# Optimization experiments

Measured on AMD Instinct MI355X. Metric: run time of the kernel, lower is better.

## Reference

```python
import jax, jax.numpy as jnp
import numpy as np

N_NODES = 100000
N_EDGES = 1600000
HIDDEN = 128
DENSE = 64
N_GRAPHS = 512


def setup_inputs() -> dict:
    key = jax.random.key(0)
    ks = jax.random.split(key, 12)
    x = jax.random.normal(ks[0], (N_NODES, 3), dtype=jnp.float32)
    edge_index = jax.random.randint(ks[1], (2, N_EDGES), 0, N_NODES, dtype=jnp.int64)
    batch = jnp.sort(jax.random.randint(ks[2], (N_NODES,), 0, N_GRAPHS, dtype=jnp.int64))
    def lin(k, fan_in, fan_out):
        s = 1.0 / np.sqrt(fan_in)
        kw, kb = jax.random.split(k)
        W = jax.random.uniform(kw, (fan_in, fan_out), jnp.float32, -s, s)
        b = jax.random.uniform(kb, (fan_out,), jnp.float32, -s, s)
        return W, b
    W0, b0 = lin(ks[3], 3, HIDDEN)
    W1, b1 = lin(ks[4], HIDDEN, HIDDEN)
    W2, b2 = lin(ks[5], HIDDEN, HIDDEN)
    Wf1, bf1 = lin(ks[6], HIDDEN, DENSE)
    Wf2, bf2 = lin(ks[7], DENSE, 1)
    return {"x": x, "edge_index": edge_index, "batch": batch,
            "W0": W0, "b0": b0, "W1": W1, "b1": b1, "W2": W2, "b2": b2,
            "Wf1": Wf1, "bf1": bf1, "Wf2": Wf2, "bf2": bf2}


def reference(x, edge_index, batch, W0, b0, W1, b1, W2, b2, Wf1, bf1, Wf2, bf2):
    N = x.shape[0]
    loop = jnp.arange(N, dtype=edge_index.dtype)
    src = jnp.concatenate([edge_index[0], loop])  # [E+N] with self-loops
    dst = jnp.concatenate([edge_index[1], loop])
    deg = jax.ops.segment_sum(jnp.ones_like(dst, dtype=x.dtype), dst, num_segments=N)
    dis = jax.lax.rsqrt(jnp.maximum(deg, 1.0))  # D^{-1/2}; self-loops => deg >= 1
    norm = dis[src] * dis[dst]  # [E+N]

    def gcn_conv(h, W, b):
        h = h @ W  # transform first (PyG GCNConv)
        msg = h[src] * norm[:, None]  # gather + edge-wise scale
        return jax.ops.segment_sum(msg, dst, num_segments=N) + b  # scatter-add

    h = jax.nn.relu(gcn_conv(x, W0, b0))
    h = jax.nn.relu(gcn_conv(h, W1, b1))
    h = jax.nn.relu(gcn_conv(h, W2, b2))

    # global mean pool over graphs
    counts = jax.ops.segment_sum(jnp.ones((N,), h.dtype), batch, num_segments=N_GRAPHS)
    pooled = jax.ops.segment_sum(h, batch, num_segments=N_GRAPHS)
    pooled = pooled / jnp.maximum(counts, 1.0)[:, None]  # [G, HIDDEN]

    out = jax.nn.relu(pooled @ Wf1 + bf1)
    return out @ Wf2 + bf2  # [G, 1]
```

## Files before the change

kernel.cpp:

```cpp
#include <hip/hip_runtime.h>

#define HID 128
#define ELLW 64
#define FP8_SCALE 16.0f
#define FP8_INV (1.0f / 16.0f)

#define NBINS 400
#define BINCAP 16
#define CHUNK_I4 512
#define BKCAP 5120
#define OVF_CAP 16384

typedef _Float16 half8 __attribute__((ext_vector_type(8)));
typedef float f32x4 __attribute__((ext_vector_type(4)));
typedef float f32x2 __attribute__((ext_vector_type(2)));
struct alignas(8) H4v { _Float16 x, y, z, w; };

__device__ __forceinline__ unsigned char f32_to_fp8(float v) {
  return (unsigned char)(__builtin_amdgcn_cvt_pk_fp8_f32(v, 0.f, 0, false) & 0xff);
}

__device__ __forceinline__ void fp8x8_to_f32(uint2 u, float* o) {
  f32x2 a = __builtin_amdgcn_cvt_pk_f32_fp8(u.x, false);
  f32x2 b = __builtin_amdgcn_cvt_pk_f32_fp8(u.x, true);
  f32x2 c = __builtin_amdgcn_cvt_pk_f32_fp8(u.y, false);
  f32x2 d = __builtin_amdgcn_cvt_pk_f32_fp8(u.y, true);
  o[0] = a[0]; o[1] = a[1]; o[2] = b[0]; o[3] = b[1];
  o[4] = c[0]; o[5] = c[1]; o[6] = d[0]; o[7] = d[1];
}

__device__ __forceinline__ void fp8x8_add(uint2 u, float* acc) {
  f32x2 a = __builtin_amdgcn_cvt_pk_f32_fp8(u.x, false);
  f32x2 b = __builtin_amdgcn_cvt_pk_f32_fp8(u.x, true);
  f32x2 c = __builtin_amdgcn_cvt_pk_f32_fp8(u.y, false);
  f32x2 d = __builtin_amdgcn_cvt_pk_f32_fp8(u.y, true);
  acc[0] += a[0]; acc[1] += a[1]; acc[2] += b[0]; acc[3] += b[1];
  acc[4] += c[0]; acc[5] += c[1]; acc[6] += d[0]; acc[7] += d[1];
}


__global__ void k_zero_ints(int* p, int n) {
  int i = blockIdx.x * blockDim.x + threadIdx.x;
  if (i < n) p[i] = 0;
}

__device__ __forceinline__ void bin_one(int s, int d, int* lcnt, unsigned* bins,
                                        int* ovfn, int2* ovf) {
  int b = d >> 8;
  int p = atomicAdd(&lcnt[b], 1);
  if (p < BINCAP) bins[b * BINCAP + p] = ((unsigned)s << 8) | (unsigned)(d & 255);
  else { int q = atomicAdd(ovfn, 1); if (q < OVF_CAP) ovf[q] = make_int2(s, d); }
}

__global__ __launch_bounds__(256) void k_binA(
    const int4* __restrict__ src4, const int4* __restrict__ dst4, int E4,
    int* bkcnt, unsigned* __restrict__ bk, int* ovfn, int2* __restrict__ ovf) {
  __shared__ unsigned bins[NBINS * BINCAP];
  __shared__ int lcnt[NBINS];
  __shared__ int gbase[NBINS];
  int t = threadIdx.x;
  for (int b = t; b < NBINS; b += 256) lcnt[b] = 0;
  __syncthreads();

  int i0 = blockIdx.x * CHUNK_I4;
  int i1 = min(i0 + CHUNK_I4, E4);
  for (int i = i0 + t; i < i1; i += 256) {
    int4 d = dst4[i];
    int4 s = src4[i];
    bin_one(s.x, d.x, lcnt, bins, ovfn, ovf);
    bin_one(s.y, d.y, lcnt, bins, ovfn, ovf);
    bin_one(s.z, d.z, lcnt, bins, ovfn, ovf);
    bin_one(s.w, d.w, lcnt, bins, ovfn, ovf);
  }
  __syncthreads();

  for (int b = t; b < NBINS; b += 256) gbase[b] = atomicAdd(&bkcnt[b], min(lcnt[b], BINCAP));
  __syncthreads();

  int wid = t >> 6, lane = t & 63;
  for (int b = wid; b < NBINS; b += 4) {
    int c = min(lcnt[b], BINCAP);
    if (lane < c) {
      int off = gbase[b] + lane;
      unsigned r = bins[b * BINCAP + lane];
      if (off < BKCAP) bk[(size_t)b * BKCAP + off] = r;
      else {
        int q = atomicAdd(ovfn, 1);
        if (q < OVF_CAP) ovf[q] = make_int2((int)(r >> 8), b * 256 + (int)(r & 255));
      }
    }
  }
}

__global__ void k_tail_ovf(const int* __restrict__ src, const int* __restrict__ dst,
                           int e0, int E, int* ovfn, int2* __restrict__ ovf) {
  int e = e0 + threadIdx.x;
  if (e < E) {
    int q = atomicAdd(ovfn, 1);
    if (q < OVF_CAP) ovf[q] = make_int2(src[e], dst[e]);
  }
}


__global__ __launch_bounds__(256) void k_ell_build2(
    const unsigned* __restrict__ bk, const int* __restrict__ bkcnt,
    int* __restrict__ ell, int* __restrict__ cnt,
    const float* __restrict__ x, float* __restrict__ dis,
    float4* __restrict__ x4, int N) {
  int b = blockIdx.x;
  int t = threadIdx.x;
  __shared__ int lcnt[256];
  lcnt[t] = 0;
  __syncthreads();
  int n = bkcnt[b]; if (n > BKCAP) n = BKCAP;
  const unsigned* my = bk + (size_t)b * BKCAP;
  for (int k = t; k < n; k += 256) {
    unsigned r = my[k];
    int d0 = (int)(r & 255);
    int s = (int)(r >> 8);
    int p = atomicAdd(&lcnt[d0], 1);
    if (p < ELLW) ell[(size_t)(b * 256 + d0) * ELLW + p] = s;
  }
  __syncthreads();
  int node = b * 256 + t;
  if (node < N) {
    int c = lcnt[t];
    cnt[node] = c;
    float s = rsqrtf((float)(c + 1));
    dis[node] = s;
    x4[node] = make_float4(s * x[node * 3 + 0], s * x[node * 3 + 1],
                           s * x[node * 3 + 2], 0.f);
  }
}

__global__ void k_ovf_build(const int2* __restrict__ ovf, const int* __restrict__ ovfn,
                            int* cnt, int* ell, const float* __restrict__ x,
                            float* dis, float4* x4) {
  int n = *ovfn; if (n > OVF_CAP) n = OVF_CAP;
  for (int k = threadIdx.x; k < n; k += blockDim.x) {
    int2 e = ovf[k];
    int p = atomicAdd(&cnt[e.y], 1);
    if (p < ELLW) ell[(size_t)e.y * ELLW + p] = e.x;
  }
  __syncthreads();
  for (int k = threadIdx.x; k < n; k += blockDim.x) {
    int d = ovf[k].y;
    float s = rsqrtf((float)(cnt[d] + 1));
    dis[d] = s;
    x4[d] = make_float4(s * x[d * 3 + 0], s * x[d * 3 + 1], s * x[d * 3 + 2], 0.f);
  }
}


__global__ void k_fill_ell1(const int* __restrict__ src, const int* __restrict__ dst,
                            int* cnt, int* ell, int E) {
  int e = blockIdx.x * blockDim.x + threadIdx.x;
  if (e < E) {
    int d = dst[e];
    int p = atomicAdd(&cnt[d], 1);
    if (p < ELLW) ell[(size_t)d * ELLW + p] = src[e];
  }
}

__global__ void k_dis_prepx(const int* __restrict__ cnt, const float* __restrict__ x,
                            float* __restrict__ dis, float4* __restrict__ x4, int N) {
  int i = blockIdx.x * blockDim.x + threadIdx.x;
  if (i >= N) return;
  float s = rsqrtf((float)(cnt[i] + 1));
  dis[i] = s;
  x4[i] = make_float4(s * x[i * 3 + 0], s * x[i * 3 + 1], s * x[i * 3 + 2], 0.f);
}


__global__ void k_prep_w16x2(const float* __restrict__ W1, const float* __restrict__ W2,
                             _Float16* __restrict__ Wt1, _Float16* __restrict__ Wt2) {
  int idx = blockIdx.x * blockDim.x + threadIdx.x;
  if (idx >= 2 * HID * HID) return;
  int which = idx >> 14;
  int r = idx & (HID * HID - 1);
  int k = r >> 7, n = r & 127;
  const float* W = which ? W2 : W1;
  _Float16* Wt = which ? Wt2 : Wt1;
  Wt[n * HID + k] = (_Float16)W[r];
}


__global__ void k_agg3(const float4* __restrict__ x4, const int* __restrict__ ell,
                       const int* __restrict__ cnt, const float* __restrict__ dis,
                       float4* __restrict__ z4, int N) {
  int i = blockIdx.x * blockDim.x + threadIdx.x;
  if (i >= N) return;
  float4 a = x4[i];
  int c = cnt[i]; if (c > ELLW) c = ELLW;
  const int* row = &ell[(size_t)i * ELLW];
  int k = 0;
  for (; k + 4 <= c; k += 4) {
    int4 s4 = *(const int4*)(row + k);
    float4 v0 = x4[s4.x], v1 = x4[s4.y], v2 = x4[s4.z], v3 = x4[s4.w];
    a.x += (v0.x + v1.x) + (v2.x + v3.x);
    a.y += (v0.y + v1.y) + (v2.y + v3.y);
    a.z += (v0.z + v1.z) + (v2.z + v3.z);
  }
  for (; k < c; ++k) {
    float4 v = x4[row[k]];
    a.x += v.x; a.y += v.y; a.z += v.z;
  }
  float s = dis[i];
  z4[i] = make_float4(s * a.x, s * a.y, s * a.z, 0.f);
}


__global__ __launch_bounds__(256) void k_l01(
    const float4* __restrict__ z4, const float* __restrict__ W0,
    const float* __restrict__ b0, const _Float16* __restrict__ wt1,
    const float* __restrict__ dis, unsigned char* __restrict__ G8, int N) {
  __shared__ _Float16 hs[64][136];
  int t = threadIdx.x;
  int base = blockIdx.x * 64;

  {
    int r = t >> 2;
    int c0 = (t & 3) * 32;
    int row = base + r;
    float4 z = make_float4(0.f, 0.f, 0.f, 0.f);
    if (row < N) z = z4[row];
#pragma unroll
    for (int c = 0; c < 32; c += 4) {
      int cc = c0 + c;
      float4 w0 = *(const float4*)&W0[0 * HID + cc];
      float4 w1 = *(const float4*)&W0[1 * HID + cc];
      float4 w2 = *(const float4*)&W0[2 * HID + cc];
      float4 bb = *(const float4*)&b0[cc];
      H4v o;
      o.x = (_Float16)fmaxf(z.x * w0.x + z.y * w1.x + z.z * w2.x + bb.x, 0.f);
      o.y = (_Float16)fmaxf(z.x * w0.y + z.y * w1.y + z.z * w2.y + bb.y, 0.f);
      o.z = (_Float16)fmaxf(z.x * w0.z + z.y * w1.z + z.z * w2.z + bb.z, 0.f);
      o.w = (_Float16)fmaxf(z.x * w0.w + z.y * w1.w + z.z * w2.w + bb.w, 0.f);
      *(H4v*)&hs[r][cc] = o;
    }
  }
  __syncthreads();

  int w = t >> 6, lane = t & 63;
  int kg = lane >> 4, ccol = lane & 15;
  int lrow = w * 16 + ccol;

  f32x4 acc[8];
#pragma unroll
  for (int nt = 0; nt < 8; ++nt) acc[nt] = (f32x4){0.f, 0.f, 0.f, 0.f};

#pragma unroll
  for (int kt = 0; kt < 4; ++kt) {
    half8 a = *(const half8*)&hs[lrow][kg * 8 + kt * 32];
#pragma unroll
    for (int nt = 0; nt < 8; ++nt) {
      half8 b = *(const half8*)(wt1 + (size_t)(nt * 16 + ccol) * HID + kg * 8 + kt * 32);
      acc[nt] = __builtin_amdgcn_mfma_f32_16x16x32_f16(a, b, acc[nt], 0, 0, 0);
    }
  }

#pragma unroll
  for (int j = 0; j < 4; ++j) {
    int row = base + w * 16 + kg * 4 + j;
    if (row < N) {
      float s = dis[row] * FP8_SCALE;
#pragma unroll
      for (int nt = 0; nt < 8; ++nt) {
        G8[(size_t)row * HID + nt * 16 + ccol] = f32_to_fp8(s * acc[nt][j]);
      }
    }
  }
}


__global__ __launch_bounds__(256) void k_g1(
    const unsigned char* __restrict__ g8, const int* __restrict__ ell,
    const int* __restrict__ cnt, const float* __restrict__ dis,
    const float* __restrict__ b, unsigned char* __restrict__ q8, int N) {
  int tid = blockIdx.x * blockDim.x + threadIdx.x;
  int i = tid >> 4;
  int q = tid & 15;
  if (i >= N) return;
  const unsigned char* gq = g8 + q * 8;

  float acc[8];
  fp8x8_to_f32(*(const uint2*)(gq + (size_t)i * HID), acc);

  int c = cnt[i]; if (c > ELLW) c = ELLW;
  const int* row = ell + (size_t)i * ELLW;
  int k = 0;
  for (; k + 4 <= c; k += 4) {
    int4 s4 = *(const int4*)(row + k);
    uint2 u0 = *(const uint2*)(gq + (size_t)s4.x * HID);
    uint2 u1 = *(const uint2*)(gq + (size_t)s4.y * HID);
    uint2 u2 = *(const uint2*)(gq + (size_t)s4.z * HID);
    uint2 u3 = *(const uint2*)(gq + (size_t)s4.w * HID);
    fp8x8_add(u0, acc);
    fp8x8_add(u1, acc);
    fp8x8_add(u2, acc);
    fp8x8_add(u3, acc);
  }
  for (; k < c; ++k) {
    fp8x8_add(*(const uint2*)(gq + (size_t)row[k] * HID), acc);
  }

  float sc = dis[i];
  float sc_in = sc * FP8_INV;
  float sc_out = sc * FP8_SCALE;
  float o[8];
#pragma unroll
  for (int j = 0; j < 8; ++j) {
    float bb = b[q * 8 + j];
    o[j] = sc_out * fmaxf(sc_in * acc[j] + bb, 0.f);
  }
  int w0 = __builtin_amdgcn_cvt_pk_fp8_f32(o[0], o[1], 0, false);
  w0 = __builtin_amdgcn_cvt_pk_fp8_f32(o[2], o[3], w0, true);
  int w1 = __builtin_amdgcn_cvt_pk_fp8_f32(o[4], o[5], 0, false);
  w1 = __builtin_amdgcn_cvt_pk_fp8_f32(o[6], o[7], w1, true);
  uint2 ov; ov.x = (unsigned)w0; ov.y = (unsigned)w1;
  *(uint2*)(q8 + (size_t)i * HID + q * 8) = ov;
}


__global__ __launch_bounds__(256) void k_gpool2(
    const unsigned char* __restrict__ q8, const int* __restrict__ ell,
    const int* __restrict__ cnt, const float* __restrict__ dis,
    const float* __restrict__ b2, const _Float16* __restrict__ wt2,
    const int* __restrict__ batch, float* __restrict__ pool, int N) {
  __shared__ _Float16 hs[16][136];
  int t = threadIdx.x;
  int base = blockIdx.x * 16;
  int gi = t >> 4, q = t & 15;
  int i = base + gi;

  if (i < N) {
    const unsigned char* gq = q8 + q * 8;
    float acc[8];
    fp8x8_to_f32(*(const uint2*)(gq + (size_t)i * HID), acc);

    int c = cnt[i]; if (c > ELLW) c = ELLW;
    const int* row = ell + (size_t)i * ELLW;
    int k = 0;
    for (; k + 4 <= c; k += 4) {
      int4 s4 = *(const int4*)(row + k);
      uint2 u0 = *(const uint2*)(gq + (size_t)s4.x * HID);
      uint2 u1 = *(const uint2*)(gq + (size_t)s4.y * HID);
      uint2 u2 = *(const uint2*)(gq + (size_t)s4.z * HID);
      uint2 u3 = *(const uint2*)(gq + (size_t)s4.w * HID);
      fp8x8_add(u0, acc);
      fp8x8_add(u1, acc);
      fp8x8_add(u2, acc);
      fp8x8_add(u3, acc);
    }
    for (; k < c; ++k) {
      fp8x8_add(*(const uint2*)(gq + (size_t)row[k] * HID), acc);
    }

    float sc = dis[i] * FP8_INV;
    half8 o;
#pragma unroll
    for (int j = 0; j < 8; ++j) o[j] = (_Float16)(sc * acc[j]);
    *(half8*)&hs[gi][q * 8] = o;
  } else {
    half8 zo;
#pragma unroll
    for (int j = 0; j < 8; ++j) zo[j] = (_Float16)0.f;
    *(half8*)&hs[gi][q * 8] = zo;
  }
  __syncthreads();

  int w = t >> 6, lane = t & 63;
  int kg = lane >> 4, rloc = lane & 15;
  f32x4 acc2[2];
  acc2[0] = (f32x4){0.f, 0.f, 0.f, 0.f};
  acc2[1] = (f32x4){0.f, 0.f, 0.f, 0.f};

#pragma unroll
  for (int kt = 0; kt < 4; ++kt) {
    half8 a = *(const half8*)&hs[rloc][kg * 8 + kt * 32];
#pragma unroll
    for (int ntl = 0; ntl < 2; ++ntl) {
      int n = (2 * w + ntl) * 16 + rloc;
      half8 bf = *(const half8*)(wt2 + (size_t)n * HID + kg * 8 + kt * 32);
      acc2[ntl] = __builtin_amdgcn_mfma_f32_16x16x32_f16(a, bf, acc2[ntl], 0, 0, 0);
    }
  }

  float v2[2][4];
#pragma unroll
  for (int ntl = 0; ntl < 2; ++ntl) {
    int col = (2 * w + ntl) * 16 + rloc;
    float bb = b2[col];
#pragma unroll
    for (int j = 0; j < 4; ++j) v2[ntl][j] = fmaxf(acc2[ntl][j] + bb, 0.f);
  }
  int brow[4];
#pragma unroll
  for (int j = 0; j < 4; ++j) {
    int row = base + kg * 4 + j;
    brow[j] = (row < N) ? batch[row] : -1;
  }
  int g0 = batch[base];
  int lastr = base + 15; if (lastr >= N) lastr = N - 1;
  int g1 = batch[lastr];

  for (int s = g0; s <= g1; ++s) {
#pragma unroll
    for (int ntl = 0; ntl < 2; ++ntl) {
      float p = 0.f;
#pragma unroll
      for (int j = 0; j < 4; ++j) p += (brow[j] == s) ? v2[ntl][j] : 0.f;
      p += __shfl_xor(p, 16);
      p += __shfl_xor(p, 32);
      if (kg == 0 && p != 0.f) {
        atomicAdd(&pool[s * HID + (2 * w + ntl) * 16 + rloc], p);
      }
    }
  }
}


__device__ __forceinline__ int lower_bound_i(const int* __restrict__ a, int n, int v) {
  int lo = 0, hi = n;
  while (lo < hi) {
    int m = (lo + hi) >> 1;
    if (a[m] < v) lo = m + 1; else hi = m;
  }
  return lo;
}

__global__ __launch_bounds__(64) void k_mlp512(
    const float* __restrict__ pool, const int* __restrict__ batch, int N,
    const float* __restrict__ Wf1, const float* __restrict__ bf1,
    const float* __restrict__ Wf2, const float* __restrict__ bf2,
    float* __restrict__ out) {
  int g = blockIdx.x;
  int lane = threadIdx.x;
  int lo = lower_bound_i(batch, N, g);
  int hi = lower_bound_i(batch, N, g + 1);
  float inv = 1.0f / fmaxf((float)(hi - lo), 1.0f);

  __shared__ float p[128];
  p[lane] = pool[g * HID + lane] * inv;
  p[lane + 64] = pool[g * HID + 64 + lane] * inv;
  __syncthreads();

  float a = bf1[lane];
  for (int k = 0; k < 128; ++k) a += p[k] * Wf1[k * 64 + lane];
  a = fmaxf(a, 0.f);
  float prod = a * Wf2[lane];
#pragma unroll
  for (int off = 32; off; off >>= 1) prod += __shfl_down(prod, off);
  if (lane == 0) out[g] = prod + bf2[0];
}


static inline size_t align256(size_t x) { return (x + 255) & ~(size_t)255; }

extern "C" void kernel_launch(void* const* d_in, const int* in_sizes, int n_in,
                              void* d_out, int out_size, void* d_ws, size_t ws_size,
                              hipStream_t stream) {
  const float* x = (const float*)d_in[0];
  const int* ei = (const int*)d_in[1];
  const int* batch = (const int*)d_in[2];
  const float* W0 = (const float*)d_in[3];
  const float* b0 = (const float*)d_in[4];
  const float* W1 = (const float*)d_in[5];
  const float* b1 = (const float*)d_in[6];
  const float* W2 = (const float*)d_in[7];
  const float* b2 = (const float*)d_in[8];
  const float* Wf1 = (const float*)d_in[9];
  const float* bf1 = (const float*)d_in[10];
  const float* Wf2 = (const float*)d_in[11];
  const float* bf2 = (const float*)d_in[12];
  float* out = (float*)d_out;

  const int N = in_sizes[0] / 3;
  const int E = in_sizes[1] / 2;
  const int Gn = out_size;
  const int nbuk = (N + 255) >> 8;

  const int* src = ei;
  const int* dst = ei + E;

  char* ws = (char*)d_ws;
  size_t o = 0;
  int* cnt = (int*)(ws + o); o = align256(o + (size_t)N * 4);
  float* dis = (float*)(ws + o); o = align256(o + (size_t)N * 4);
  float4* x4 = (float4*)(ws + o); o = align256(o + (size_t)N * 16);
  float4* z4 = (float4*)(ws + o); o = align256(o + (size_t)N * 16);
  int* ell = (int*)(ws + o); o = align256(o + (size_t)N * ELLW * 4);
  unsigned char* g8a = (unsigned char*)(ws + o); o = align256(o + (size_t)N * HID);
  unsigned char* q8 = (unsigned char*)(ws + o); o = align256(o + (size_t)N * HID);
  _Float16* wt1 = (_Float16*)(ws + o); o = align256(o + (size_t)HID * HID * 2);
  _Float16* wt2 = (_Float16*)(ws + o); o = align256(o + (size_t)HID * HID * 2);
  size_t zero_base = o;
  int* bkcnt = (int*)(ws + o); o = align256(o + (size_t)(NBINS + 1) * 4);
  int* ovfn = bkcnt + NBINS;
  float* pool = (float*)(ws + o); o = align256(o + (size_t)Gn * HID * 4);
  size_t zero_bytes = o - zero_base;
  unsigned* bk = (unsigned*)(ws + o); o = align256(o + (size_t)NBINS * BKCAP * 4);
  int2* ovf = (int2*)(ws + o); o = align256(o + (size_t)OVF_CAP * 8);

  const int BS = 256;
  int gN = (N + BS - 1) / BS;
  int gN16 = (int)(((long long)N * 16 + BS - 1) / BS);
  int gW2 = (2 * HID * HID + BS - 1) / BS;
  int zn = (int)(zero_bytes / 4);

  k_zero_ints<<<(zn + BS - 1) / BS, BS, 0, stream>>>((int*)(ws + zero_base), zn);

  bool vec4ok = (E % 4 == 0) && (((uintptr_t)src & 15) == 0) && (((uintptr_t)dst & 15) == 0);
  if (nbuk <= NBINS) {
    int E4 = E / 4;
    if (E4 > 0 && vec4ok) {
      k_binA<<<(E4 + CHUNK_I4 - 1) / CHUNK_I4, 256, 0, stream>>>(
          (const int4*)src, (const int4*)dst, E4, bkcnt, bk, ovfn, ovf);
      if (E % 4) k_tail_ovf<<<1, 64, 0, stream>>>(src, dst, E4 * 4, E, ovfn, ovf);
    } else {
      k_tail_ovf<<<1, 256, 0, stream>>>(src, dst, 0, E, ovfn, ovf);
    }
    k_ell_build2<<<nbuk, 256, 0, stream>>>(bk, bkcnt, ell, cnt, x, dis, x4, N);
    k_ovf_build<<<1, 256, 0, stream>>>(ovf, ovfn, cnt, ell, x, dis, x4);
  } else {
    k_zero_ints<<<gN, BS, 0, stream>>>(cnt, N);
    k_fill_ell1<<<(E + BS - 1) / BS, BS, 0, stream>>>(src, dst, cnt, ell, E);
    k_dis_prepx<<<gN, BS, 0, stream>>>(cnt, x, dis, x4, N);
  }

  k_prep_w16x2<<<gW2, BS, 0, stream>>>(W1, W2, wt1, wt2);

  k_agg3<<<gN, BS, 0, stream>>>(x4, ell, cnt, dis, z4, N);

  k_l01<<<(N + 63) / 64, 256, 0, stream>>>(z4, W0, b0, wt1, dis, g8a, N);

  k_g1<<<gN16, BS, 0, stream>>>(g8a, ell, cnt, dis, b1, q8, N);

  k_gpool2<<<(N + 15) / 16, 256, 0, stream>>>(q8, ell, cnt, dis, b2, wt2, batch, pool, N);

  k_mlp512<<<Gn, 64, 0, stream>>>(pool, batch, N, Wf1, bf1, Wf2, bf2, out);
}
```

Measured before the change: 234.9 us.

## Rebalance per-node thread mapping in aggregation kernels with wider fp8 gathers

The first-layer aggregation now uses four threads per node with strided neighbor loops and a shuffle reduction, instead of one thread per node. The fp8 gather kernels for layers 1 and 2 use eight threads per node, each loading 16 bytes, instead of sixteen threads loading 8 bytes. The pool kernel processes 32 nodes per block, with each wave computing four MFMA column tiles. The aim is to spread irregular degree work more evenly for the 3-wide features and to halve the number of gather instructions per row. The cost is more registers per thread and fewer threads in flight for the 128-wide layers.

```diff
diff --git a/kernel.cpp b/kernel.cpp
--- a/kernel.cpp
+++ b/kernel.cpp
@@ -18,15 +18,6 @@
 
 __device__ __forceinline__ unsigned char f32_to_fp8(float v) {
   return (unsigned char)(__builtin_amdgcn_cvt_pk_fp8_f32(v, 0.f, 0, false) & 0xff);
-}
-
-__device__ __forceinline__ void fp8x8_to_f32(uint2 u, float* o) {
-  f32x2 a = __builtin_amdgcn_cvt_pk_f32_fp8(u.x, false);
-  f32x2 b = __builtin_amdgcn_cvt_pk_f32_fp8(u.x, true);
-  f32x2 c = __builtin_amdgcn_cvt_pk_f32_fp8(u.y, false);
-  f32x2 d = __builtin_amdgcn_cvt_pk_f32_fp8(u.y, true);
-  o[0] = a[0]; o[1] = a[1]; o[2] = b[0]; o[3] = b[1];
-  o[4] = c[0]; o[5] = c[1]; o[6] = d[0]; o[7] = d[1];
 }
 
 __device__ __forceinline__ void fp8x8_add(uint2 u, float* acc) {
@@ -36,6 +27,26 @@
   f32x2 d = __builtin_amdgcn_cvt_pk_f32_fp8(u.y, true);
   acc[0] += a[0]; acc[1] += a[1]; acc[2] += b[0]; acc[3] += b[1];
   acc[4] += c[0]; acc[5] += c[1]; acc[6] += d[0]; acc[7] += d[1];
+}
+
+__device__ __forceinline__ void fp8x16_to_f32(uint4 u, float* o) {
+  f32x2 a = __builtin_amdgcn_cvt_pk_f32_fp8(u.x, false);
+  f32x2 b = __builtin_amdgcn_cvt_pk_f32_fp8(u.x, true);
+  f32x2 c = __builtin_amdgcn_cvt_pk_f32_fp8(u.y, false);
+  f32x2 d = __builtin_amdgcn_cvt_pk_f32_fp8(u.y, true);
+  f32x2 e = __builtin_amdgcn_cvt_pk_f32_fp8(u.z, false);
+  f32x2 f = __builtin_amdgcn_cvt_pk_f32_fp8(u.z, true);
+  f32x2 g = __builtin_amdgcn_cvt_pk_f32_fp8(u.w, false);
+  f32x2 h = __builtin_amdgcn_cvt_pk_f32_fp8(u.w, true);
+  o[0]=a[0]; o[1]=a[1]; o[2]=b[0]; o[3]=b[1];
+  o[4]=c[0]; o[5]=c[1]; o[6]=d[0]; o[7]=d[1];
+  o[8]=e[0]; o[9]=e[1]; o[10]=f[0]; o[11]=f[1];
+  o[12]=g[0]; o[13]=g[1]; o[14]=h[0]; o[15]=h[1];
+}
+
+__device__ __forceinline__ void fp8x16_add(uint4 u, float* acc) {
+  fp8x8_add(make_uint2(u.x, u.y), acc);
+  fp8x8_add(make_uint2(u.z, u.w), acc + 8);
 }
 
 
@@ -188,25 +199,27 @@
 __global__ void k_agg3(const float4* __restrict__ x4, const int* __restrict__ ell,
                        const int* __restrict__ cnt, const float* __restrict__ dis,
                        float4* __restrict__ z4, int N) {
-  int i = blockIdx.x * blockDim.x + threadIdx.x;
+  int tid = blockIdx.x * blockDim.x + threadIdx.x;
+  int i = tid >> 2, sub = tid & 3;
   if (i >= N) return;
-  float4 a = x4[i];
+  float ax = 0.f, ay = 0.f, az = 0.f;
   int c = cnt[i]; if (c > ELLW) c = ELLW;
   const int* row = &ell[(size_t)i * ELLW];
-  int k = 0;
-  for (; k + 4 <= c; k += 4) {
-    int4 s4 = *(const int4*)(row + k);
-    float4 v0 = x4[s4.x], v1 = x4[s4.y], v2 = x4[s4.z], v3 = x4[s4.w];
-    a.x += (v0.x + v1.x) + (v2.x + v3.x);
-    a.y += (v0.y + v1.y) + (v2.y + v3.y);
-    a.z += (v0.z + v1.z) + (v2.z + v3.z);
-  }
-  for (; k < c; ++k) {
+  for (int k = sub; k < c; k += 4) {
     float4 v = x4[row[k]];
-    a.x += v.x; a.y += v.y; a.z += v.z;
-  }
-  float s = dis[i];
-  z4[i] = make_float4(s * a.x, s * a.y, s * a.z, 0.f);
+    ax += v.x; ay += v.y; az += v.z;
+  }
+  if (sub == 0) {
+    float4 v = x4[i];
+    ax += v.x; ay += v.y; az += v.z;
+  }
+  ax += __shfl_xor(ax, 1); ax += __shfl_xor(ax, 2);
+  ay += __shfl_xor(ay, 1); ay += __shfl_xor(ay, 2);
+  az += __shfl_xor(az, 1); az += __shfl_xor(az, 2);
+  if (sub == 0) {
+    float s = dis[i];
+    z4[i] = make_float4(s * ax, s * ay, s * az, 0.f);
+  }
 }
 
 
@@ -278,47 +291,52 @@
     const int* __restrict__ cnt, const float* __restrict__ dis,
     const float* __restrict__ b, unsigned char* __restrict__ q8, int N) {
   int tid = blockIdx.x * blockDim.x + threadIdx.x;
-  int i = tid >> 4;
-  int q = tid & 15;
+  int i = tid >> 3;
+  int q = tid & 7;
   if (i >= N) return;
-  const unsigned char* gq = g8 + q * 8;
-
-  float acc[8];
-  fp8x8_to_f32(*(const uint2*)(gq + (size_t)i * HID), acc);
+  const unsigned char* gq = g8 + q * 16;
+
+  float acc[16];
+  fp8x16_to_f32(*(const uint4*)(gq + (size_t)i * HID), acc);
 
   int c = cnt[i]; if (c > ELLW) c = ELLW;
   const int* row = ell + (size_t)i * ELLW;
   int k = 0;
   for (; k + 4 <= c; k += 4) {
     int4 s4 = *(const int4*)(row + k);
-    uint2 u0 = *(const uint2*)(gq + (size_t)s4.x * HID);
-    uint2 u1 = *(const uint2*)(gq + (size_t)s4.y * HID);
-    uint2 u2 = *(const uint2*)(gq + (size_t)s4.z * HID);
-    uint2 u3 = *(const uint2*)(gq + (size_t)s4.w * HID);
-    fp8x8_add(u0, acc);
-    fp8x8_add(u1, acc);
-    fp8x8_add(u2, acc);
-    fp8x8_add(u3, acc);
+    uint4 u0 = *(const uint4*)(gq + (size_t)s4.x * HID);
+    uint4 u1 = *(const uint4*)(gq + (size_t)s4.y * HID);
+    uint4 u2 = *(const uint4*)(gq + (size_t)s4.z * HID);
+    uint4 u3 = *(const uint4*)(gq + (size_t)s4.w * HID);
+    fp8x16_add(u0, acc);
+    fp8x16_add(u1, acc);
+    fp8x16_add(u2, acc);
+    fp8x16_add(u3, acc);
   }
   for (; k < c; ++k) {
-    fp8x8_add(*(const uint2*)(gq + (size_t)row[k] * HID), acc);
+    fp8x16_add(*(const uint4*)(gq + (size_t)row[k] * HID), acc);
   }
 
   float sc = dis[i];
   float sc_in = sc * FP8_INV;
   float sc_out = sc * FP8_SCALE;
-  float o[8];
-#pragma unroll
-  for (int j = 0; j < 8; ++j) {
-    float bb = b[q * 8 + j];
+  float o[16];
+#pragma unroll
+  for (int j = 0; j < 16; ++j) {
+    float bb = b[q * 16 + j];
     o[j] = sc_out * fmaxf(sc_in * acc[j] + bb, 0.f);
   }
+  uint4 ov;
   int w0 = __builtin_amdgcn_cvt_pk_fp8_f32(o[0], o[1], 0, false);
   w0 = __builtin_amdgcn_cvt_pk_fp8_f32(o[2], o[3], w0, true);
   int w1 = __builtin_amdgcn_cvt_pk_fp8_f32(o[4], o[5], 0, false);
   w1 = __builtin_amdgcn_cvt_pk_fp8_f32(o[6], o[7], w1, true);
-  uint2 ov; ov.x = (unsigned)w0; ov.y = (unsigned)w1;
-  *(uint2*)(q8 + (size_t)i * HID + q * 8) = ov;
+  int w2 = __builtin_amdgcn_cvt_pk_fp8_f32(o[8], o[9], 0, false);
+  w2 = __builtin_amdgcn_cvt_pk_fp8_f32(o[10], o[11], w2, true);
+  int w3 = __builtin_amdgcn_cvt_pk_fp8_f32(o[12], o[13], 0, false);
+  w3 = __builtin_amdgcn_cvt_pk_fp8_f32(o[14], o[15], w3, true);
+  ov.x = (unsigned)w0; ov.y = (unsigned)w1; ov.z = (unsigned)w2; ov.w = (unsigned)w3;
+  *(uint4*)(q8 + (size_t)i * HID + q * 16) = ov;
 }
 
 
@@ -327,69 +345,77 @@
     const int* __restrict__ cnt, const float* __restrict__ dis,
     const float* __restrict__ b2, const _Float16* __restrict__ wt2,
     const int* __restrict__ batch, float* __restrict__ pool, int N) {
-  __shared__ _Float16 hs[16][136];
+  __shared__ _Float16 hs[32][136];
   int t = threadIdx.x;
-  int base = blockIdx.x * 16;
-  int gi = t >> 4, q = t & 15;
+  int base = blockIdx.x * 32;
+  int gi = t >> 3, q = t & 7;
   int i = base + gi;
 
   if (i < N) {
-    const unsigned char* gq = q8 + q * 8;
-    float acc[8];
-    fp8x8_to_f32(*(const uint2*)(gq + (size_t)i * HID), acc);
+    const unsigned char* gq = q8 + q * 16;
+    float acc[16];
+    fp8x16_to_f32(*(const uint4*)(gq + (size_t)i * HID), acc);
 
     int c = cnt[i]; if (c > ELLW) c = ELLW;
     const int* row = ell + (size_t)i * ELLW;
     int k = 0;
     for (; k + 4 <= c; k += 4) {
       int4 s4 = *(const int4*)(row + k);
-      uint2 u0 = *(const uint2*)(gq + (size_t)s4.x * HID);
-      uint2 u1 = *(const uint2*)(gq + (size_t)s4.y * HID);
-      uint2 u2 = *(const uint2*)(gq + (size_t)s4.z * HID);
-      uint2 u3 = *(const uint2*)(gq + (size_t)s4.w * HID);
-      fp8x8_add(u0, acc);
-      fp8x8_add(u1, acc);
-      fp8x8_add(u2, acc);
-      fp8x8_add(u3, acc);
+      uint4 u0 = *(const uint4*)(gq + (size_t)s4.x * HID);
+      uint4 u1 = *(const uint4*)(gq + (size_t)s4.y * HID);
+      uint4 u2 = *(const uint4*)(gq + (size_t)s4.z * HID);
+      uint4 u3 = *(const uint4*)(gq + (size_t)s4.w * HID);
+      fp8x16_add(u0, acc);
+      fp8x16_add(u1, acc);
+      fp8x16_add(u2, acc);
+      fp8x16_add(u3, acc);
     }
     for (; k < c; ++k) {
-      fp8x8_add(*(const uint2*)(gq + (size_t)row[k] * HID), acc);
+      fp8x16_add(*(const uint4*)(gq + (size_t)row[k] * HID), acc);
     }
 
     float sc = dis[i] * FP8_INV;
-    half8 o;
-#pragma unroll
-    for (int j = 0; j < 8; ++j) o[j] = (_Float16)(sc * acc[j]);
-    *(half8*)&hs[gi][q * 8] = o;
+    half8 o0, o1;
+#pragma unroll
+    for (int j = 0; j < 8; ++j) {
+      o0[j] = (_Float16)(sc * acc[j]);
+      o1[j] = (_Float16)(sc * acc[8 + j]);
+    }
+    *(half8*)&hs[gi][q * 16] = o0;
+    *(half8*)&hs[gi][q * 16 + 8] = o1;
   } else {
     half8 zo;
 #pragma unroll
     for (int j = 0; j < 8; ++j) zo[j] = (_Float16)0.f;
-    *(half8*)&hs[gi][q * 8] = zo;
+    *(half8*)&hs[gi][q * 16] = zo;
+    *(half8*)&hs[gi][q * 16 + 8] = zo;
   }
   __syncthreads();
 
   int w = t >> 6, lane = t & 63;
   int kg = lane >> 4, rloc = lane & 15;
-  f32x4 acc2[2];
-  acc2[0] = (f32x4){0.f, 0.f, 0.f, 0.f};
-  acc2[1] = (f32x4){0.f, 0.f, 0.f, 0.f};
+  int tw = w >> 1, ch = w & 1;
+  int rbase = base + tw * 16;
+
+  f32x4 acc2[4];
+#pragma unroll
+  for (int ntl = 0; ntl < 4; ++ntl) acc2[ntl] = (f32x4){0.f, 0.f, 0.f, 0.f};
 
 #pragma unroll
   for (int kt = 0; kt < 4; ++kt) {
-    half8 a = *(const half8*)&hs[rloc][kg * 8 + kt * 32];
-#pragma unroll
-    for (int ntl = 0; ntl < 2; ++ntl) {
-      int n = (2 * w + ntl) * 16 + rloc;
+    half8 a = *(const half8*)&hs[tw * 16 + rloc][kg * 8 + kt * 32];
+#pragma unroll
+    for (int ntl = 0; ntl < 4; ++ntl) {
+      int n = (ch * 4 + ntl) * 16 + rloc;
       half8 bf = *(const half8*)(wt2 + (size_t)n * HID + kg * 8 + kt * 32);
       acc2[ntl] = __builtin_amdgcn_mfma_f32_16x16x32_f16(a, bf, acc2[ntl], 0, 0, 0);
     }
   }
 
-  float v2[2][4];
-#pragma unroll
-  for (int ntl = 0; ntl < 2; ++ntl) {
-    int col = (2 * w + ntl) * 16 + rloc;
+  float v2[4][4];
+#pragma unroll
+  for (int ntl = 0; ntl < 4; ++ntl) {
+    int col = (ch * 4 + ntl) * 16 + rloc;
     float bb = b2[col];
 #pragma unroll
     for (int j = 0; j < 4; ++j) v2[ntl][j] = fmaxf(acc2[ntl][j] + bb, 0.f);
@@ -397,23 +423,24 @@
   int brow[4];
 #pragma unroll
   for (int j = 0; j < 4; ++j) {
-    int row = base + kg * 4 + j;
+    int row = rbase + kg * 4 + j;
     brow[j] = (row < N) ? batch[row] : -1;
   }
-  int g0 = batch[base];
-  int lastr = base + 15; if (lastr >= N) lastr = N - 1;
+  int r0c = (rbase < N) ? rbase : (N - 1);
+  int lastr = rbase + 15; if (lastr >= N) lastr = N - 1;
+  int g0 = batch[r0c];
   int g1 = batch[lastr];
 
   for (int s = g0; s <= g1; ++s) {
 #pragma unroll
-    for (int ntl = 0; ntl < 2; ++ntl) {
+    for (int ntl = 0; ntl < 4; ++ntl) {
       float p = 0.f;
 #pragma unroll
       for (int j = 0; j < 4; ++j) p += (brow[j] == s) ? v2[ntl][j] : 0.f;
       p += __shfl_xor(p, 16);
       p += __shfl_xor(p, 32);
       if (kg == 0 && p != 0.f) {
-        atomicAdd(&pool[s * HID + (2 * w + ntl) * 16 + rloc], p);
+        atomicAdd(&pool[s * HID + (ch * 4 + ntl) * 16 + rloc], p);
       }
     }
   }
@@ -504,7 +531,8 @@
 
   const int BS = 256;
   int gN = (N + BS - 1) / BS;
-  int gN16 = (int)(((long long)N * 16 + BS - 1) / BS);
+  int gN4 = (int)(((long long)N * 4 + BS - 1) / BS);
+  int gN8 = (int)(((long long)N * 8 + BS - 1) / BS);
   int gW2 = (2 * HID * HID + BS - 1) / BS;
   int zn = (int)(zero_bytes / 4);
 
@@ -530,13 +558,13 @@
 
   k_prep_w16x2<<<gW2, BS, 0, stream>>>(W1, W2, wt1, wt2);
 
-  k_agg3<<<gN, BS, 0, stream>>>(x4, ell, cnt, dis, z4, N);
+  k_agg3<<<gN4, BS, 0, stream>>>(x4, ell, cnt, dis, z4, N);
 
   k_l01<<<(N + 63) / 64, 256, 0, stream>>>(z4, W0, b0, wt1, dis, g8a, N);
 
-  k_g1<<<gN16, BS, 0, stream>>>(g8a, ell, cnt, dis, b1, q8, N);
-
-  k_gpool2<<<(N + 15) / 16, 256, 0, stream>>>(q8, ell, cnt, dis, b2, wt2, batch, pool, N);
+  k_g1<<<gN8, BS, 0, stream>>>(g8a, ell, cnt, dis, b1, q8, N);
+
+  k_gpool2<<<(N + 31) / 32, 256, 0, stream>>>(q8, ell, cnt, dis, b2, wt2, batch, pool, N);
 
   k_mlp512<<<Gn, 64, 0, stream>>>(pool, batch, N, Wf1, bf1, Wf2, bf2, out);
 }
```

New measurement: 235.5 us. Within noise of the previous version (+0.3%).

## Aggregate first layer from dst buckets with LDS atomics; stage fp8 output for coalesced stores

Applied to the files above, without the earlier changes.

The first-layer 3-wide aggregation now runs directly over the destination-binned edge buckets. It accumulates into shared-memory atomics per 256-node bucket, plus a separate pass that adds overflow edges with global atomics, replacing the ELL row gather kernel. k_l01 now writes its fp8 outputs into LDS first and then stores 16-byte coalesced rows, instead of scattered byte stores. The trade-offs are LDS atomic contention, float atomic ordering nondeterminism, and extra syncthreads.

```diff
diff --git a/kernel.cpp b/kernel.cpp
--- a/kernel.cpp
+++ b/kernel.cpp
@@ -152,6 +152,51 @@
 }
 
 
+__global__ __launch_bounds__(256) void k_aggB(
+    const unsigned* __restrict__ bk, const int* __restrict__ bkcnt,
+    const float4* __restrict__ x4, const float* __restrict__ dis,
+    float4* __restrict__ z4, int N) {
+  __shared__ float sx[256], sy[256], sz[256];
+  int b = blockIdx.x;
+  int t = threadIdx.x;
+  sx[t] = 0.f; sy[t] = 0.f; sz[t] = 0.f;
+  __syncthreads();
+  int n = bkcnt[b]; if (n > BKCAP) n = BKCAP;
+  const unsigned* my = bk + (size_t)b * BKCAP;
+  for (int k = t; k < n; k += 256) {
+    unsigned r = my[k];
+    int d0 = (int)(r & 255);
+    float4 v = x4[r >> 8];
+    atomicAdd(&sx[d0], v.x);
+    atomicAdd(&sy[d0], v.y);
+    atomicAdd(&sz[d0], v.z);
+  }
+  __syncthreads();
+  int node = b * 256 + t;
+  if (node < N) {
+    float4 self = x4[node];
+    float s = dis[node];
+    z4[node] = make_float4(s * (sx[t] + self.x), s * (sy[t] + self.y),
+                           s * (sz[t] + self.z), 0.f);
+  }
+}
+
+__global__ void k_ovf_agg(const int2* __restrict__ ovf, const int* __restrict__ ovfn,
+                          const float* __restrict__ dis, const float4* __restrict__ x4,
+                          float4* z4) {
+  int n = *ovfn; if (n > OVF_CAP) n = OVF_CAP;
+  for (int k = threadIdx.x; k < n; k += blockDim.x) {
+    int2 e = ovf[k];
+    float4 v = x4[e.x];
+    float s = dis[e.y];
+    float* zp = (float*)&z4[e.y];
+    atomicAdd(zp + 0, s * v.x);
+    atomicAdd(zp + 1, s * v.y);
+    atomicAdd(zp + 2, s * v.z);
+  }
+}
+
+
 __global__ void k_fill_ell1(const int* __restrict__ src, const int* __restrict__ dst,
                             int* cnt, int* ell, int E) {
   int e = blockIdx.x * blockDim.x + threadIdx.x;
@@ -170,20 +215,6 @@
   dis[i] = s;
   x4[i] = make_float4(s * x[i * 3 + 0], s * x[i * 3 + 1], s * x[i * 3 + 2], 0.f);
 }
-
-
-__global__ void k_prep_w16x2(const float* __restrict__ W1, const float* __restrict__ W2,
-                             _Float16* __restrict__ Wt1, _Float16* __restrict__ Wt2) {
-  int idx = blockIdx.x * blockDim.x + threadIdx.x;
-  if (idx >= 2 * HID * HID) return;
-  int which = idx >> 14;
-  int r = idx & (HID * HID - 1);
-  int k = r >> 7, n = r & 127;
-  const float* W = which ? W2 : W1;
-  _Float16* Wt = which ? Wt2 : Wt1;
-  Wt[n * HID + k] = (_Float16)W[r];
-}
-
 
 __global__ void k_agg3(const float4* __restrict__ x4, const int* __restrict__ ell,
                        const int* __restrict__ cnt, const float* __restrict__ dis,
@@ -210,6 +241,19 @@
 }
 
 
+__global__ void k_prep_w16x2(const float* __restrict__ W1, const float* __restrict__ W2,
+                             _Float16* __restrict__ Wt1, _Float16* __restrict__ Wt2) {
+  int idx = blockIdx.x * blockDim.x + threadIdx.x;
+  if (idx >= 2 * HID * HID) return;
+  int which = idx >> 14;
+  int r = idx & (HID * HID - 1);
+  int k = r >> 7, n = r & 127;
+  const float* W = which ? W2 : W1;
+  _Float16* Wt = which ? Wt2 : Wt1;
+  Wt[n * HID + k] = (_Float16)W[r];
+}
+
+
 __global__ __launch_bounds__(256) void k_l01(
     const float4* __restrict__ z4, const float* __restrict__ W0,
     const float* __restrict__ b0, const _Float16* __restrict__ wt1,
@@ -258,16 +302,29 @@
       acc[nt] = __builtin_amdgcn_mfma_f32_16x16x32_f16(a, b, acc[nt], 0, 0, 0);
     }
   }
-
+  __syncthreads();
+
+  unsigned char* bytebuf = (unsigned char*)&hs[0][0];
 #pragma unroll
   for (int j = 0; j < 4; ++j) {
-    int row = base + w * 16 + kg * 4 + j;
+    int rl = w * 16 + kg * 4 + j;
+    int row = base + rl;
+    float s = dis[(row < N) ? row : (N - 1)] * FP8_SCALE;
+#pragma unroll
+    for (int nt = 0; nt < 8; ++nt) {
+      bytebuf[rl * 144 + nt * 16 + ccol] = f32_to_fp8(s * acc[nt][j]);
+    }
+  }
+  __syncthreads();
+
+#pragma unroll
+  for (int half = 0; half < 2; ++half) {
+    int rl = (t >> 3) + half * 32;
+    int seg = t & 7;
+    int row = base + rl;
     if (row < N) {
-      float s = dis[row] * FP8_SCALE;
-#pragma unroll
-      for (int nt = 0; nt < 8; ++nt) {
-        G8[(size_t)row * HID + nt * 16 + ccol] = f32_to_fp8(s * acc[nt][j]);
-      }
+      uint4 v = *(const uint4*)&bytebuf[rl * 144 + seg * 16];
+      *(uint4*)&G8[(size_t)row * HID + seg * 16] = v;
     }
   }
 }
@@ -522,16 +579,17 @@
     }
     k_ell_build2<<<nbuk, 256, 0, stream>>>(bk, bkcnt, ell, cnt, x, dis, x4, N);
     k_ovf_build<<<1, 256, 0, stream>>>(ovf, ovfn, cnt, ell, x, dis, x4);
+    k_aggB<<<nbuk, 256, 0, stream>>>(bk, bkcnt, x4, dis, z4, N);
+    k_ovf_agg<<<1, 256, 0, stream>>>(ovf, ovfn, dis, x4, z4);
   } else {
     k_zero_ints<<<gN, BS, 0, stream>>>(cnt, N);
     k_fill_ell1<<<(E + BS - 1) / BS, BS, 0, stream>>>(src, dst, cnt, ell, E);
     k_dis_prepx<<<gN, BS, 0, stream>>>(cnt, x, dis, x4, N);
+    k_agg3<<<gN, BS, 0, stream>>>(x4, ell, cnt, dis, z4, N);
   }
 
   k_prep_w16x2<<<gW2, BS, 0, stream>>>(W1, W2, wt1, wt2);
 
-  k_agg3<<<gN, BS, 0, stream>>>(x4, ell, cnt, dis, z4, N);
-
   k_l01<<<(N + 63) / 64, 256, 0, stream>>>(z4, W0, b0, wt1, dis, g8a, N);
 
   k_g1<<<gN16, BS, 0, stream>>>(g8a, ell, cnt, dis, b1, q8, N);
```

Result: slower. 253.3 us (+7.9%).

## Split layer-0 aggregation across four lanes per node and stage FP8 stores through LDS

Applied to the files above, without the earlier changes.

The first-layer 3-wide aggregation now gives each node four threads, one float component each, with an 8-way unrolled gather. This exposes more memory-level parallelism than one thread per node doing float4 gathers. Separately, k_l01 writes its FP8 outputs into shared memory and then copies them out as coalesced 16-byte rows, replacing scattered single-byte global stores. The cost is extra threads doing redundant index loads, plus additional barriers and LDS traffic in k_l01.

```diff
diff --git a/kernel.cpp b/kernel.cpp
--- a/kernel.cpp
+++ b/kernel.cpp
@@ -172,6 +172,45 @@
 }
 
 
+__global__ __launch_bounds__(256) void k_aggv(
+    const float* __restrict__ x4f, const int* __restrict__ ell,
+    const int* __restrict__ cnt, const float* __restrict__ dis,
+    float* __restrict__ z4f, int N) {
+  int tid = blockIdx.x * blockDim.x + threadIdx.x;
+  int i = tid >> 2, q = tid & 3;
+  if (i >= N) return;
+
+  float acc = x4f[i * 4 + q];
+  int c = cnt[i]; if (c > ELLW) c = ELLW;
+  const int* row = ell + (size_t)i * ELLW;
+  int k = 0;
+  for (; k + 8 <= c; k += 8) {
+    int4 sa = *(const int4*)(row + k);
+    int4 sb = *(const int4*)(row + k + 4);
+    float v0 = x4f[sa.x * 4 + q];
+    float v1 = x4f[sa.y * 4 + q];
+    float v2 = x4f[sa.z * 4 + q];
+    float v3 = x4f[sa.w * 4 + q];
+    float v4 = x4f[sb.x * 4 + q];
+    float v5 = x4f[sb.y * 4 + q];
+    float v6 = x4f[sb.z * 4 + q];
+    float v7 = x4f[sb.w * 4 + q];
+    acc += ((v0 + v1) + (v2 + v3)) + ((v4 + v5) + (v6 + v7));
+  }
+  for (; k + 4 <= c; k += 4) {
+    int4 s4 = *(const int4*)(row + k);
+    float v0 = x4f[s4.x * 4 + q];
+    float v1 = x4f[s4.y * 4 + q];
+    float v2 = x4f[s4.z * 4 + q];
+    float v3 = x4f[s4.w * 4 + q];
+    acc += (v0 + v1) + (v2 + v3);
+  }
+  for (; k < c; ++k) acc += x4f[row[k] * 4 + q];
+
+  z4f[i * 4 + q] = dis[i] * acc;
+}
+
+
 __global__ void k_prep_w16x2(const float* __restrict__ W1, const float* __restrict__ W2,
                              _Float16* __restrict__ Wt1, _Float16* __restrict__ Wt2) {
   int idx = blockIdx.x * blockDim.x + threadIdx.x;
@@ -182,31 +221,6 @@
   const float* W = which ? W2 : W1;
   _Float16* Wt = which ? Wt2 : Wt1;
   Wt[n * HID + k] = (_Float16)W[r];
-}
-
-
-__global__ void k_agg3(const float4* __restrict__ x4, const int* __restrict__ ell,
-                       const int* __restrict__ cnt, const float* __restrict__ dis,
-                       float4* __restrict__ z4, int N) {
-  int i = blockIdx.x * blockDim.x + threadIdx.x;
-  if (i >= N) return;
-  float4 a = x4[i];
-  int c = cnt[i]; if (c > ELLW) c = ELLW;
-  const int* row = &ell[(size_t)i * ELLW];
-  int k = 0;
-  for (; k + 4 <= c; k += 4) {
-    int4 s4 = *(const int4*)(row + k);
-    float4 v0 = x4[s4.x], v1 = x4[s4.y], v2 = x4[s4.z], v3 = x4[s4.w];
-    a.x += (v0.x + v1.x) + (v2.x + v3.x);
-    a.y += (v0.y + v1.y) + (v2.y + v3.y);
-    a.z += (v0.z + v1.z) + (v2.z + v3.z);
-  }
-  for (; k < c; ++k) {
-    float4 v = x4[row[k]];
-    a.x += v.x; a.y += v.y; a.z += v.z;
-  }
-  float s = dis[i];
-  z4[i] = make_float4(s * a.x, s * a.y, s * a.z, 0.f);
 }
 
 
@@ -258,16 +272,29 @@
       acc[nt] = __builtin_amdgcn_mfma_f32_16x16x32_f16(a, b, acc[nt], 0, 0, 0);
     }
   }
-
+  __syncthreads();
+
+  unsigned char* bytebuf = (unsigned char*)&hs[0][0];
 #pragma unroll
   for (int j = 0; j < 4; ++j) {
-    int row = base + w * 16 + kg * 4 + j;
+    int rl = w * 16 + kg * 4 + j;
+    int row = base + rl;
+    float s = dis[(row < N) ? row : (N - 1)] * FP8_SCALE;
+#pragma unroll
+    for (int nt = 0; nt < 8; ++nt) {
+      bytebuf[rl * 144 + nt * 16 + ccol] = f32_to_fp8(s * acc[nt][j]);
+    }
+  }
+  __syncthreads();
+
+#pragma unroll
+  for (int half = 0; half < 2; ++half) {
+    int rl = (t >> 3) + half * 32;
+    int seg = t & 7;
+    int row = base + rl;
     if (row < N) {
-      float s = dis[row] * FP8_SCALE;
-#pragma unroll
-      for (int nt = 0; nt < 8; ++nt) {
-        G8[(size_t)row * HID + nt * 16 + ccol] = f32_to_fp8(s * acc[nt][j]);
-      }
+      uint4 v = *(const uint4*)&bytebuf[rl * 144 + seg * 16];
+      *(uint4*)&G8[(size_t)row * HID + seg * 16] = v;
     }
   }
 }
@@ -504,6 +531,7 @@
 
   const int BS = 256;
   int gN = (N + BS - 1) / BS;
+  int gN4 = (int)(((long long)N * 4 + BS - 1) / BS);
   int gN16 = (int)(((long long)N * 16 + BS - 1) / BS);
   int gW2 = (2 * HID * HID + BS - 1) / BS;
   int zn = (int)(zero_bytes / 4);
@@ -528,10 +556,10 @@
     k_dis_prepx<<<gN, BS, 0, stream>>>(cnt, x, dis, x4, N);
   }
 
+  k_aggv<<<gN4, BS, 0, stream>>>((const float*)x4, ell, cnt, dis, (float*)z4, N);
+
   k_prep_w16x2<<<gW2, BS, 0, stream>>>(W1, W2, wt1, wt2);
 
-  k_agg3<<<gN, BS, 0, stream>>>(x4, ell, cnt, dis, z4, N);
-
   k_l01<<<(N + 63) / 64, 256, 0, stream>>>(z4, W0, b0, wt1, dis, g8a, N);
 
   k_g1<<<gN16, BS, 0, stream>>>(g8a, ell, cnt, dis, b1, q8, N);
```

Result: faster. 230.2 us (-2.0%).
